# Kernel tuning notes

Measured on AMD Instinct MI355X. Metric: run time of the kernel, lower is better.

Reference implementation:

```python
import jax, jax.numpy as jnp
import numpy as np

B, S, D, H = 4, 1024, 1024, 16
DEPTH = D // H


def setup_inputs() -> dict:
    key = jax.random.key(0)
    ks = jax.random.split(key, 13)
    inp = {
        'query': jax.random.normal(ks[0], (B, S, D), dtype=jnp.float32),
        'key': jax.random.normal(ks[1], (B, S, D), dtype=jnp.float32),
        'value': jax.random.normal(ks[2], (B, S, D), dtype=jnp.float32),
        'mask': jax.random.bernoulli(ks[3], 0.1, (B, S, S)),
    }
    scale = 1.0 / np.sqrt(D)
    inp['wq_w'] = jax.random.uniform(ks[4], (D, D), jnp.float32, -scale, scale)
    inp['wq_b'] = jax.random.uniform(ks[5], (D,), jnp.float32, -scale, scale)
    inp['wk_w'] = jax.random.uniform(ks[6], (D, D), jnp.float32, -scale, scale)
    inp['wk_b'] = jax.random.uniform(ks[7], (D,), jnp.float32, -scale, scale)
    inp['wv_w'] = jax.random.uniform(ks[8], (D, D), jnp.float32, -scale, scale)
    inp['wv_b'] = jax.random.uniform(ks[9], (D,), jnp.float32, -scale, scale)
    inp['fc_w'] = jax.random.uniform(ks[10], (D, D), jnp.float32, -scale, scale)
    inp['fc_b'] = jax.random.uniform(ks[11], (D,), jnp.float32, -scale, scale)
    return inp


def _split_heads(x):
    # [B,S,D] -> [B,H,S,depth]
    b, s, _ = x.shape
    return x.reshape(b, s, H, DEPTH).transpose(0, 2, 1, 3)


def reference(query, key, value, mask, wq_w, wq_b, wk_w, wk_b, wv_w, wv_b, fc_w, fc_b):
    q = _split_heads(query @ wq_w.T + wq_b)
    k = _split_heads(key @ wk_w.T + wk_b)
    v = _split_heads(value @ wv_w.T + wv_b)
    scores = jnp.einsum('bhqd,bhkd->bhqk', q, k) / jnp.sqrt(jnp.float32(DEPTH))
    scores = jnp.where(mask[:, None, :, :], jnp.float32(-1e9), scores)
    attn = jax.nn.softmax(scores, axis=-1)
    out = jnp.einsum('bhqk,bhkd->bhqd', attn, v)  # [B,H,S,depth]
    out = out.transpose(0, 2, 1, 3).reshape(query.shape[0], -1, D)
    return out @ fc_w.T + fc_b
```

## Files before the change

kernel.cpp:

```cpp
#include <hip/hip_runtime.h>
#include <hip/hip_bf16.h>


typedef __bf16 bf16x8 __attribute__((ext_vector_type(8)));
typedef __bf16 bf16x4 __attribute__((ext_vector_type(4)));
typedef float  f32x4  __attribute__((ext_vector_type(4)));
typedef float  f32x16 __attribute__((ext_vector_type(16)));

typedef const __attribute__((address_space(1))) void* gptr_t;
typedef __attribute__((address_space(3))) void* lptr_t;

#define MFMA16(a, b, c) __builtin_amdgcn_mfma_f32_16x16x32_bf16((a), (b), (c), 0, 0, 0)
#define MFMA32(a, b, c) __builtin_amdgcn_mfma_f32_32x32x16_bf16((a), (b), (c), 0, 0, 0)

__device__ __forceinline__ void gload_lds16(const void* g, void* l) {
  __builtin_amdgcn_global_load_lds((gptr_t)g, (lptr_t)l, 16, 0, 0);
}

__device__ __forceinline__ unsigned pack2(float a, float b) {
  union { __bf16 h[2]; unsigned u; } x;
  x.h[0] = (__bf16)a; x.h[1] = (__bf16)b; return x.u;
}

__device__ __forceinline__ bf16x8 mkfrag(unsigned a, unsigned b, unsigned c, unsigned d) {
  union { unsigned w[4]; bf16x8 v; } x;
  x.w[0] = a; x.w[1] = b; x.w[2] = c; x.w[3] = d; return x.v;
}

__global__ void detect_mask(const unsigned char* m, int* flag) {
  __shared__ int s1[4], s23[4];
  int tid = threadIdx.x;
  uint4 v = ((const uint4*)m)[tid];
  unsigned x0 = v.x, x1 = v.y, x2 = v.z, x3 = v.w;
  unsigned c1  = (x0 & 0x0000ff00u) | (x1 & 0x0000ff00u) | (x2 & 0x0000ff00u) | (x3 & 0x0000ff00u);
  unsigned c23 = (x0 & 0xffff0000u) | (x1 & 0xffff0000u) | (x2 & 0xffff0000u) | (x3 & 0xffff0000u);
  unsigned long long b1 = __ballot(c1 != 0), b23 = __ballot(c23 != 0);
  if ((tid & 63) == 0) { s1[tid >> 6] = (b1 != 0); s23[tid >> 6] = (b23 != 0); }
  __syncthreads();
  if (tid == 0) {
    int a1 = s1[0] | s1[1] | s1[2] | s1[3];
    int a23 = s23[0] | s23[1] | s23[2] | s23[3];
    *flag = a1 ? 1 : (a23 ? 2 : 0);
  }
}

__global__ void pack_mask(const void* m, const int* flag, unsigned int* out) {
  size_t i = (size_t)blockIdx.x * 256 + threadIdx.x;
  int f = *flag;
  bool v;
  if (f == 1)      v = ((const unsigned char*)m)[i] != 0;
  else if (f == 2) v = ((const float*)m)[i] != 0.0f;
  else             v = ((const int*)m)[i] != 0;
  unsigned long long bal = __ballot(v);
  int lane = threadIdx.x & 63;
  if ((lane & 31) == 0) out[i >> 5] = (unsigned int)(bal >> (lane & 32));
}

__global__ void cvt_all(const float* q, const float* k, const float* v,
                        const float* w0, const float* w1, const float* w2, const float* w3,
                        __bf16* oq, __bf16* ok, __bf16* ov,
                        __bf16* o0, __bf16* o1, __bf16* o2, __bf16* o3) {
  int bid = blockIdx.x;
  const float* in; __bf16* out; int sub;
  if (bid < 12288) {
    int w = bid >> 12; sub = bid & 4095;
    in = w == 0 ? q : w == 1 ? k : v;
    out = w == 0 ? oq : w == 1 ? ok : ov;
  } else {
    int w = (bid - 12288) >> 10; sub = (bid - 12288) & 1023;
    in = w == 0 ? w0 : w == 1 ? w1 : w == 2 ? w2 : w3;
    out = w == 0 ? o0 : w == 1 ? o1 : w == 2 ? o2 : o3;
  }
  size_t i = (size_t)sub * 256 + threadIdx.x;
  float4 vv = ((const float4*)in)[i];
  bf16x4 o; o[0] = (__bf16)vv.x; o[1] = (__bf16)vv.y; o[2] = (__bf16)vv.z; o[3] = (__bf16)vv.w;
  ((bf16x4*)out)[i] = o;
}

__global__ __launch_bounds__(256, 2)
void gemm_qkv(const __bf16* __restrict__ qb, const __bf16* __restrict__ kb,
              const __bf16* __restrict__ vb,
              const __bf16* __restrict__ wq, const __bf16* __restrict__ wk,
              const __bf16* __restrict__ wv,
              const float* __restrict__ bq, const float* __restrict__ bk,
              const float* __restrict__ bv,
              __bf16* __restrict__ Qp, __bf16* __restrict__ Kp, __bf16* __restrict__ Vt) {
  __shared__ __bf16 As[2][128 * 64];
  __shared__ __bf16 Bs[2][128 * 64];
  const int bm = blockIdx.x;
  const int bnall = blockIdx.y;
  const int which = bnall >> 3;
  const int bn = bnall & 7;
  const __bf16* A = which == 0 ? qb : which == 1 ? kb : vb;
  const __bf16* W = which == 0 ? wq : which == 1 ? wk : wv;
  const float* bias = which == 0 ? bq : which == 1 ? bk : bv;

  const int tid = threadIdx.x, wave = tid >> 6, lane = tid & 63;
  const int wr = wave >> 1, wc = wave & 1;
  const int rl = lane >> 3, c8 = lane & 7;
  f32x4 acc[4][4] = {};

#define QKV_STAGE(bb, kt)                                                             \
  {                                                                                   \
    _Pragma("unroll")                                                                 \
    for (int i = 0; i < 4; ++i) {                                                     \
      int row = wave * 32 + i * 8 + rl;                                               \
      int sw = (c8 ^ (row & 7)) << 3;                                                 \
      gload_lds16(A + (size_t)(bm * 128 + row) * 1024 + (kt) * 64 + sw,               \
                  &As[bb][(wave * 32 + i * 8) * 64]);                                 \
      gload_lds16(W + (size_t)(bn * 128 + row) * 1024 + (kt) * 64 + sw,               \
                  &Bs[bb][(wave * 32 + i * 8) * 64]);                                 \
    }                                                                                 \
  }

  QKV_STAGE(0, 0);
  __syncthreads();
  int buf = 0;
  for (int kt = 0; kt < 16; ++kt) {
    if (kt < 15) QKV_STAGE(buf ^ 1, kt + 1);
#pragma unroll
    for (int k32 = 0; k32 < 2; ++k32) {
      bf16x8 af[4], bfr[4];
#pragma unroll
      for (int mi = 0; mi < 4; ++mi) {
        int row = wr * 64 + mi * 16 + (lane & 15);
        af[mi] = *(const bf16x8*)(&As[buf][row * 64 + (((k32 * 4 + (lane >> 4)) ^ (row & 7)) << 3)]);
      }
#pragma unroll
      for (int ni = 0; ni < 4; ++ni) {
        int row = wc * 64 + ni * 16 + (lane & 15);
        bfr[ni] = *(const bf16x8*)(&Bs[buf][row * 64 + (((k32 * 4 + (lane >> 4)) ^ (row & 7)) << 3)]);
      }
#pragma unroll
      for (int mi = 0; mi < 4; ++mi)
#pragma unroll
        for (int ni = 0; ni < 4; ++ni)
          acc[mi][ni] = MFMA16(af[mi], bfr[ni], acc[mi][ni]);
    }
    __syncthreads();
    buf ^= 1;
  }
  const int r0 = (lane >> 4) * 4, cl = lane & 15;
  const float osc = (which == 0) ? 0.18033688011112042f : 1.0f;
  __bf16* Onat = which == 0 ? Qp : Kp;
#pragma unroll
  for (int ni = 0; ni < 4; ++ni) {
    int col = bn * 128 + wc * 64 + ni * 16 + cl;
    float bvv = bias[col];
#pragma unroll
    for (int mi = 0; mi < 4; ++mi) {
      int rowb = bm * 128 + wr * 64 + mi * 16 + r0;
      if (which < 2) {
#pragma unroll
        for (int r = 0; r < 4; ++r)
          Onat[(size_t)(rowb + r) * 1024 + col] = (__bf16)((acc[mi][ni][r] + bvv) * osc);
      } else {
        int bb = rowb >> 10, s0 = rowb & 1023, hh = col >> 6, d = col & 63;
        bf16x4 ov;
#pragma unroll
        for (int r = 0; r < 4; ++r) ov[r] = (__bf16)(acc[mi][ni][r] + bvv);
        *(bf16x4*)(Vt + (((size_t)(bb * 16 + hh) * 64 + d) << 10) + s0) = ov;
      }
    }
  }
}

__global__ __launch_bounds__(256, 2)
void gemm_fc(const __bf16* __restrict__ A, const __bf16* __restrict__ W,
             const float* __restrict__ bias, float* __restrict__ C) {
  __shared__ __bf16 As[2][128 * 64];
  __shared__ __bf16 Bs[2][128 * 64];
  const int bm = blockIdx.x, bn = blockIdx.y;
  const int tid = threadIdx.x, wave = tid >> 6, lane = tid & 63;
  const int wr = wave >> 1, wc = wave & 1;
  const int rl = lane >> 3, c8 = lane & 7;
  f32x4 acc[4][4] = {};

#define FC_STAGE(bb, kt)                                                              \
  {                                                                                   \
    _Pragma("unroll")                                                                 \
    for (int i = 0; i < 4; ++i) {                                                     \
      int row = wave * 32 + i * 8 + rl;                                               \
      int sw = (c8 ^ (row & 7)) << 3;                                                 \
      gload_lds16(A + (size_t)(bm * 128 + row) * 1024 + (kt) * 64 + sw,               \
                  &As[bb][(wave * 32 + i * 8) * 64]);                                 \
      gload_lds16(W + (size_t)(bn * 128 + row) * 1024 + (kt) * 64 + sw,               \
                  &Bs[bb][(wave * 32 + i * 8) * 64]);                                 \
    }                                                                                 \
  }

  FC_STAGE(0, 0);
  __syncthreads();
  int buf = 0;
  for (int kt = 0; kt < 16; ++kt) {
    if (kt < 15) FC_STAGE(buf ^ 1, kt + 1);
#pragma unroll
    for (int k32 = 0; k32 < 2; ++k32) {
      bf16x8 af[4], bfr[4];
#pragma unroll
      for (int mi = 0; mi < 4; ++mi) {
        int row = wr * 64 + mi * 16 + (lane & 15);
        af[mi] = *(const bf16x8*)(&As[buf][row * 64 + (((k32 * 4 + (lane >> 4)) ^ (row & 7)) << 3)]);
      }
#pragma unroll
      for (int ni = 0; ni < 4; ++ni) {
        int row = wc * 64 + ni * 16 + (lane & 15);
        bfr[ni] = *(const bf16x8*)(&Bs[buf][row * 64 + (((k32 * 4 + (lane >> 4)) ^ (row & 7)) << 3)]);
      }
#pragma unroll
      for (int mi = 0; mi < 4; ++mi)
#pragma unroll
        for (int ni = 0; ni < 4; ++ni)
          acc[mi][ni] = MFMA16(af[mi], bfr[ni], acc[mi][ni]);
    }
    __syncthreads();
    buf ^= 1;
  }
  const int r0 = (lane >> 4) * 4, cl = lane & 15;
#pragma unroll
  for (int ni = 0; ni < 4; ++ni) {
    int col = bn * 128 + wc * 64 + ni * 16 + cl;
    float bvv = bias[col];
#pragma unroll
    for (int mi = 0; mi < 4; ++mi) {
      int rowb = bm * 128 + wr * 64 + mi * 16 + r0;
#pragma unroll
      for (int r = 0; r < 4; ++r)
        C[(size_t)(rowb + r) * 1024 + col] = acc[mi][ni][r] + bvv;
    }
  }
}

__global__ __launch_bounds__(256)
void attn32(const __bf16* __restrict__ Qp, const __bf16* __restrict__ Kp,
            const __bf16* __restrict__ Vt, const unsigned int* __restrict__ mp,
            __bf16* __restrict__ O) {
  __shared__ __bf16 Ks[2][64 * 64];
  __shared__ __bf16 Vs[2][64 * 64];
  const int tid = threadIdx.x, wave = tid >> 6, lane = tid & 63;
  const int lo5 = lane & 31, hi = lane >> 5;
  const int bx = blockIdx.x;
  const int qt = bx & 7, h = (bx >> 3) & 15, b = bx >> 7;
  const int qrow = qt * 128 + wave * 32 + lo5;

  const int srow = tid >> 3;
  const int sgx = ((tid & 7) ^ (srow & 7)) << 3;

#define ATTN_STAGE(bb, kt)                                                            \
  {                                                                                   \
    _Pragma("unroll")                                                                 \
    for (int i = 0; i < 2; ++i) {                                                     \
      gload_lds16(Kp + (size_t)(b * 1024 + (kt) * 64 + i * 32 + srow) * 1024          \
                     + h * 64 + sgx,                                                  \
                  &Ks[bb][i * 2048 + wave * 512]);                                    \
      gload_lds16(Vt + (size_t)((b * 16 + h) * 64 + i * 32 + srow) * 1024             \
                     + (kt) * 64 + sgx,                                               \
                  &Vs[bb][i * 2048 + wave * 512]);                                    \
    }                                                                                 \
  }

  bf16x8 qf[4];
  const __bf16* qb = Qp + ((size_t)(b * 1024 + qrow)) * 1024 + h * 64 + hi * 8;
#pragma unroll
  for (int m = 0; m < 4; ++m) qf[m] = *(const bf16x8*)(qb + m * 16);

  bf16x8 onesf;
#pragma unroll
  for (int i = 0; i < 8; ++i) onesf[i] = (__bf16)1.0f;

  f32x16 oacc0 = {}, oacc1 = {}, oaccD = {};
  const uint2* mrow = ((const uint2*)mp) + ((size_t)(b * 1024 + qrow)) * 16;
  const int x = lo5 & 7;

  ATTN_STAGE(0, 0);
  uint2 mwc = mrow[0];
  __syncthreads();
  int buf = 0;
  for (int kt = 0; kt < 16; ++kt) {
    if (kt < 15) ATTN_STAGE(buf ^ 1, kt + 1);
    uint2 mwn = mwc;
    if (kt < 15) mwn = mrow[kt + 1];
#pragma unroll
    for (int sub = 0; sub < 2; ++sub) {
      f32x16 s = {};
#pragma unroll
      for (int m = 0; m < 4; ++m) {
        bf16x8 kf = *(const bf16x8*)(&Ks[buf][(sub * 32 + lo5) * 64 + (((2 * m + hi) ^ x) << 3)]);
        s = MFMA32(kf, qf[m], s);
      }
      unsigned w32 = sub == 0 ? mwc.x : mwc.y;
      unsigned nw = ~(w32 >> (hi * 4));
      float p[16];
#pragma unroll
      for (int r = 0; r < 16; ++r) {
        float e = __builtin_amdgcn_exp2f(s[r]);
        unsigned keep = (unsigned)__builtin_amdgcn_sbfe((int)nw, (unsigned)((r & 3) + 8 * (r >> 2)), 1u);
        p[r] = __uint_as_float(__float_as_uint(e) & keep);
      }
      unsigned own[8];
#pragma unroll
      for (int u = 0; u < 4; ++u) {
        own[2 * u]     = pack2(p[4 * u],     p[4 * u + 1]);
        own[2 * u + 1] = pack2(p[4 * u + 2], p[4 * u + 3]);
      }
#pragma unroll
      for (int sf = 0; sf < 2; ++sf) {
        unsigned a0 = own[4 * sf + 0], b0 = own[4 * sf + 2];
        unsigned a1 = own[4 * sf + 1], b1 = own[4 * sf + 3];
        asm volatile("v_permlane32_swap_b32 %0, %1" : "+v"(a0), "+v"(b0));
        asm volatile("v_permlane32_swap_b32 %0, %1" : "+v"(a1), "+v"(b1));
        bf16x8 pa = mkfrag(a0, a1, b0, b1);
        int g = ((sub * 4 + sf * 2 + hi) ^ x) << 3;
        bf16x8 vf0 = *(const bf16x8*)(&Vs[buf][lo5 * 64 + g]);
        bf16x8 vf1 = *(const bf16x8*)(&Vs[buf][(lo5 + 32) * 64 + g]);
        oacc0 = MFMA32(pa, vf0, oacc0);
        oacc1 = MFMA32(pa, vf1, oacc1);
        oaccD = MFMA32(pa, onesf, oaccD);
      }
    }
    __syncthreads();
    buf ^= 1;
    mwc = mwn;
  }

  const size_t orow0 = (size_t)(b * 1024 + qt * 128 + wave * 32);
#pragma unroll
  for (int r = 0; r < 16; ++r) {
    int cr = (r & 3) + 8 * (r >> 2) + 4 * hi;
    float iv = __builtin_amdgcn_rcpf(oaccD[r]);
    __bf16* op = O + (orow0 + cr) * 1024 + h * 64 + lo5;
    op[0]  = (__bf16)(oacc0[r] * iv);
    op[32] = (__bf16)(oacc1[r] * iv);
  }
}

extern "C" void kernel_launch(void* const* d_in, const int* in_sizes, int n_in,
                              void* d_out, int out_size, void* d_ws, size_t ws_size,
                              hipStream_t stream) {
  const float* query = (const float*)d_in[0];
  const float* key   = (const float*)d_in[1];
  const float* value = (const float*)d_in[2];
  const void*  mask  = d_in[3];
  const float* wq_w  = (const float*)d_in[4];
  const float* wq_b  = (const float*)d_in[5];
  const float* wk_w  = (const float*)d_in[6];
  const float* wk_b  = (const float*)d_in[7];
  const float* wv_w  = (const float*)d_in[8];
  const float* wv_b  = (const float*)d_in[9];
  const float* fc_w  = (const float*)d_in[10];
  const float* fc_b  = (const float*)d_in[11];

  char* ws = (char*)d_ws;
  __bf16* qb  = (__bf16*)ws;
  __bf16* kb  = qb  + 4194304;
  __bf16* vb  = kb  + 4194304;
  __bf16* wqb = vb  + 4194304;
  __bf16* wkb = wqb + 1048576;
  __bf16* wvb = wkb + 1048576;
  __bf16* fcb = wvb + 1048576;
  __bf16* Qp  = fcb + 1048576;
  __bf16* Kp  = Qp  + 4194304;
  __bf16* Vt  = Kp  + 4194304;
  __bf16* Ob  = Vt  + 4194304;
  unsigned int* mpk = (unsigned int*)(Ob + 4194304);
  int* flag = (int*)(mpk + 131072);

  detect_mask<<<1, 256, 0, stream>>>((const unsigned char*)mask, flag);
  pack_mask<<<16384, 256, 0, stream>>>(mask, flag, mpk);
  cvt_all<<<16384, 256, 0, stream>>>(query, key, value, wq_w, wk_w, wv_w, fc_w,
                                     qb, kb, vb, wqb, wkb, wvb, fcb);
  dim3 g1(32, 24);
  gemm_qkv<<<g1, 256, 0, stream>>>(qb, kb, vb, wqb, wkb, wvb, wq_b, wk_b, wv_b, Qp, Kp, Vt);
  attn32<<<512, 256, 0, stream>>>(Qp, Kp, Vt, mpk, Ob);
  dim3 g2(32, 8);
  gemm_fc<<<g2, 256, 0, stream>>>(Ob, fcb, fc_b, (float*)d_out);
}
```

Measured before the change: 236.6 us.

## Rewrite QKV GEMM as 256x256 tile, 8-wave kernel with phased prefetch

Replaces the 128x128, 4-wave QKV projection GEMM with a 256x256 tile handled by 8 waves. The K loop is split into four compute phases, and each phase issues part of the next tile's global-to-LDS loads, with explicit barriers, sched_barrier and setprio around the MFMA bursts. The aim is more data reuse per block and better overlap of loads with MFMA work. The grid shrinks to 192 blocks, fewer than the CU count, so occupancy drops, and LDS use rises to 128KB per block.

```diff
diff --git a/kernel.cpp b/kernel.cpp
--- a/kernel.cpp
+++ b/kernel.cpp
@@ -77,79 +77,108 @@
   ((bf16x4*)out)[i] = o;
 }
 
-__global__ __launch_bounds__(256, 2)
-void gemm_qkv(const __bf16* __restrict__ qb, const __bf16* __restrict__ kb,
-              const __bf16* __restrict__ vb,
-              const __bf16* __restrict__ wq, const __bf16* __restrict__ wk,
-              const __bf16* __restrict__ wv,
-              const float* __restrict__ bq, const float* __restrict__ bk,
-              const float* __restrict__ bv,
-              __bf16* __restrict__ Qp, __bf16* __restrict__ Kp, __bf16* __restrict__ Vt) {
-  __shared__ __bf16 As[2][128 * 64];
-  __shared__ __bf16 Bs[2][128 * 64];
+__global__ __launch_bounds__(512, 2)
+void gemm_qkv8(const __bf16* __restrict__ qb, const __bf16* __restrict__ kb,
+               const __bf16* __restrict__ vb,
+               const __bf16* __restrict__ wq, const __bf16* __restrict__ wk,
+               const __bf16* __restrict__ wv,
+               const float* __restrict__ bq, const float* __restrict__ bk,
+               const float* __restrict__ bv,
+               __bf16* __restrict__ Qp, __bf16* __restrict__ Kp, __bf16* __restrict__ Vt) {
+  __shared__ __bf16 As[2][256 * 64];
+  __shared__ __bf16 Bs[2][256 * 64];
   const int bm = blockIdx.x;
   const int bnall = blockIdx.y;
-  const int which = bnall >> 3;
-  const int bn = bnall & 7;
+  const int which = bnall >> 2;
+  const int bnl = bnall & 3;
   const __bf16* A = which == 0 ? qb : which == 1 ? kb : vb;
   const __bf16* W = which == 0 ? wq : which == 1 ? wk : wv;
   const float* bias = which == 0 ? bq : which == 1 ? bk : bv;
 
   const int tid = threadIdx.x, wave = tid >> 6, lane = tid & 63;
-  const int wr = wave >> 1, wc = wave & 1;
-  const int rl = lane >> 3, c8 = lane & 7;
-  f32x4 acc[4][4] = {};
-
-#define QKV_STAGE(bb, kt)                                                             \
-  {                                                                                   \
-    _Pragma("unroll")                                                                 \
-    for (int i = 0; i < 4; ++i) {                                                     \
-      int row = wave * 32 + i * 8 + rl;                                               \
-      int sw = (c8 ^ (row & 7)) << 3;                                                 \
-      gload_lds16(A + (size_t)(bm * 128 + row) * 1024 + (kt) * 64 + sw,               \
-                  &As[bb][(wave * 32 + i * 8) * 64]);                                 \
-      gload_lds16(W + (size_t)(bn * 128 + row) * 1024 + (kt) * 64 + sw,               \
-                  &Bs[bb][(wave * 32 + i * 8) * 64]);                                 \
-    }                                                                                 \
-  }
-
-  QKV_STAGE(0, 0);
-  __syncthreads();
-  int buf = 0;
-  for (int kt = 0; kt < 16; ++kt) {
-    if (kt < 15) QKV_STAGE(buf ^ 1, kt + 1);
-#pragma unroll
-    for (int k32 = 0; k32 < 2; ++k32) {
-      bf16x8 af[4], bfr[4];
-#pragma unroll
-      for (int mi = 0; mi < 4; ++mi) {
-        int row = wr * 64 + mi * 16 + (lane & 15);
-        af[mi] = *(const bf16x8*)(&As[buf][row * 64 + (((k32 * 4 + (lane >> 4)) ^ (row & 7)) << 3)]);
-      }
-#pragma unroll
-      for (int ni = 0; ni < 4; ++ni) {
-        int row = wc * 64 + ni * 16 + (lane & 15);
-        bfr[ni] = *(const bf16x8*)(&Bs[buf][row * 64 + (((k32 * 4 + (lane >> 4)) ^ (row & 7)) << 3)]);
-      }
-#pragma unroll
-      for (int mi = 0; mi < 4; ++mi)
-#pragma unroll
-        for (int ni = 0; ni < 4; ++ni)
-          acc[mi][ni] = MFMA16(af[mi], bfr[ni], acc[mi][ni]);
-    }
-    __syncthreads();
-    buf ^= 1;
-  }
-  const int r0 = (lane >> 4) * 4, cl = lane & 15;
+  const int wr = wave >> 2, wc = wave & 3;
+  const int l15 = lane & 15, l4 = lane >> 4;
+  const int srow = tid >> 3;
+  const int sgw = ((tid & 7) ^ (srow & 7)) << 3;
+  f32x4 acc[8][4] = {};
+
+#define STAGE_HALF(bb, u, hp)                                                   \
+  {                                                                             \
+    _Pragma("unroll")                                                           \
+    for (int i_ = 0; i_ < 2; ++i_) {                                            \
+      int row_ = ((hp) & 1) * 128 + i_ * 64 + srow;                             \
+      if ((hp) < 2)                                                             \
+        gload_lds16(A + (size_t)(bm * 256 + row_) * 1024 + (u) * 64 + sgw,      \
+                    &As[bb][(((hp) & 1) * 128 + i_ * 64 + wave * 8) * 64]);     \
+      else                                                                      \
+        gload_lds16(W + (size_t)(bnl * 256 + row_) * 1024 + (u) * 64 + sgw,     \
+                    &Bs[bb][(((hp) & 1) * 128 + i_ * 64 + wave * 8) * 64]);     \
+    }                                                                           \
+  }
+
+#define PHASE(curb, mh, nh, DOSTAGE)                                            \
+  {                                                                             \
+    bf16x8 af_[4][2], bf_[2][2];                                                \
+    _Pragma("unroll")                                                           \
+    for (int j_ = 0; j_ < 4; ++j_) {                                            \
+      int row_ = wr * 128 + ((mh) * 4 + j_) * 16 + l15;                         \
+      _Pragma("unroll")                                                         \
+      for (int k_ = 0; k_ < 2; ++k_)                                            \
+        af_[j_][k_] = *(const bf16x8*)(&As[curb][row_ * 64 +                    \
+                          (((k_ * 4 + l4) ^ (row_ & 7)) << 3)]);                \
+    }                                                                           \
+    _Pragma("unroll")                                                           \
+    for (int n_ = 0; n_ < 2; ++n_) {                                            \
+      int row_ = wc * 64 + ((nh) * 2 + n_) * 16 + l15;                          \
+      _Pragma("unroll")                                                         \
+      for (int k_ = 0; k_ < 2; ++k_)                                            \
+        bf_[n_][k_] = *(const bf16x8*)(&Bs[curb][row_ * 64 +                    \
+                          (((k_ * 4 + l4) ^ (row_ & 7)) << 3)]);                \
+    }                                                                           \
+    DOSTAGE;                                                                    \
+    __builtin_amdgcn_s_barrier();                                               \
+    __builtin_amdgcn_sched_barrier(0);                                          \
+    __builtin_amdgcn_s_setprio(1);                                              \
+    _Pragma("unroll")                                                           \
+    for (int k_ = 0; k_ < 2; ++k_)                                              \
+      _Pragma("unroll")                                                         \
+      for (int j_ = 0; j_ < 4; ++j_)                                            \
+        _Pragma("unroll")                                                       \
+        for (int n_ = 0; n_ < 2; ++n_)                                          \
+          acc[(mh) * 4 + j_][(nh) * 2 + n_] =                                   \
+              MFMA16(af_[j_][k_], bf_[n_][k_], acc[(mh) * 4 + j_][(nh) * 2 + n_]); \
+    __builtin_amdgcn_s_setprio(0);                                              \
+    __builtin_amdgcn_s_barrier();                                               \
+    __builtin_amdgcn_sched_barrier(0);                                          \
+  }
+
+  STAGE_HALF(0, 0, 0); STAGE_HALF(0, 0, 1); STAGE_HALF(0, 0, 2); STAGE_HALF(0, 0, 3);
+  int cur = 0;
+#pragma unroll 1
+  for (int u = 0; u < 16; ++u) {
+    const int nu = u < 15 ? u + 1 : 15;
+    const int oth = cur ^ 1;
+    STAGE_HALF(oth, nu, 0);
+    asm volatile("s_waitcnt vmcnt(2)" ::: "memory");
+    __builtin_amdgcn_s_barrier();
+    __builtin_amdgcn_sched_barrier(0);
+    PHASE(cur, 0, 0, {});
+    PHASE(cur, 1, 0, STAGE_HALF(oth, nu, 1));
+    PHASE(cur, 0, 1, STAGE_HALF(oth, nu, 2));
+    PHASE(cur, 1, 1, STAGE_HALF(oth, nu, 3));
+    cur ^= 1;
+  }
+
+  const int r0 = l4 * 4, cl = l15;
   const float osc = (which == 0) ? 0.18033688011112042f : 1.0f;
   __bf16* Onat = which == 0 ? Qp : Kp;
 #pragma unroll
   for (int ni = 0; ni < 4; ++ni) {
-    int col = bn * 128 + wc * 64 + ni * 16 + cl;
+    int col = bnl * 256 + wc * 64 + ni * 16 + cl;
     float bvv = bias[col];
 #pragma unroll
-    for (int mi = 0; mi < 4; ++mi) {
-      int rowb = bm * 128 + wr * 64 + mi * 16 + r0;
+    for (int mi = 0; mi < 8; ++mi) {
+      int rowb = bm * 256 + wr * 128 + mi * 16 + r0;
       if (which < 2) {
 #pragma unroll
         for (int r = 0; r < 4; ++r)
@@ -163,6 +192,8 @@
       }
     }
   }
+#undef STAGE_HALF
+#undef PHASE
 }
 
 __global__ __launch_bounds__(256, 2)
@@ -369,8 +400,8 @@
   pack_mask<<<16384, 256, 0, stream>>>(mask, flag, mpk);
   cvt_all<<<16384, 256, 0, stream>>>(query, key, value, wq_w, wk_w, wv_w, fc_w,
                                      qb, kb, vb, wqb, wkb, wvb, fcb);
-  dim3 g1(32, 24);
-  gemm_qkv<<<g1, 256, 0, stream>>>(qb, kb, vb, wqb, wkb, wvb, wq_b, wk_b, wv_b, Qp, Kp, Vt);
+  dim3 g1(16, 12);
+  gemm_qkv8<<<g1, 512, 0, stream>>>(qb, kb, vb, wqb, wkb, wvb, wq_b, wk_b, wv_b, Qp, Kp, Vt);
   attn32<<<512, 256, 0, stream>>>(Qp, Kp, Vt, mpk, Ob);
   dim3 g2(32, 8);
   gemm_fc<<<g2, 256, 0, stream>>>(Ob, fcb, fc_b, (float*)d_out);
```

After: 240.7 us. About the same (+1.8%).

## Restructure GEMM main loops with two-stage-ahead prefetch and explicit waitcnt barriers

Applied to the files above, without the earlier changes.

Both projection GEMMs now issue loads two K-tiles ahead instead of one. They wait with explicit vmcnt counts rather than a full __syncthreads, so one tile's global-to-LDS loads stay in flight across the barrier. Each iteration reads all LDS fragments up front, barriers, refills the freed buffer, then runs the MFMAs at raised wave priority. The aim is to hide global memory latency behind compute. In exchange the schedule leans on hand-placed waitcnt values and sched_barriers, which are fragile if the load count per stage changes.

```diff
diff --git a/kernel.cpp b/kernel.cpp
--- a/kernel.cpp
+++ b/kernel.cpp
@@ -78,13 +78,13 @@
 }
 
 __global__ __launch_bounds__(256, 2)
-void gemm_qkv(const __bf16* __restrict__ qb, const __bf16* __restrict__ kb,
-              const __bf16* __restrict__ vb,
-              const __bf16* __restrict__ wq, const __bf16* __restrict__ wk,
-              const __bf16* __restrict__ wv,
-              const float* __restrict__ bq, const float* __restrict__ bk,
-              const float* __restrict__ bv,
-              __bf16* __restrict__ Qp, __bf16* __restrict__ Kp, __bf16* __restrict__ Vt) {
+void gemm_qkv2(const __bf16* __restrict__ qb, const __bf16* __restrict__ kb,
+               const __bf16* __restrict__ vb,
+               const __bf16* __restrict__ wq, const __bf16* __restrict__ wk,
+               const __bf16* __restrict__ wv,
+               const float* __restrict__ bq, const float* __restrict__ bk,
+               const float* __restrict__ bv,
+               __bf16* __restrict__ Qp, __bf16* __restrict__ Kp, __bf16* __restrict__ Vt) {
   __shared__ __bf16 As[2][128 * 64];
   __shared__ __bf16 Bs[2][128 * 64];
   const int bm = blockIdx.x;
@@ -97,50 +97,65 @@
 
   const int tid = threadIdx.x, wave = tid >> 6, lane = tid & 63;
   const int wr = wave >> 1, wc = wave & 1;
+  const int l15 = lane & 15, l4 = lane >> 4;
   const int rl = lane >> 3, c8 = lane & 7;
   f32x4 acc[4][4] = {};
 
 #define QKV_STAGE(bb, kt)                                                             \
   {                                                                                   \
     _Pragma("unroll")                                                                 \
-    for (int i = 0; i < 4; ++i) {                                                     \
-      int row = wave * 32 + i * 8 + rl;                                               \
-      int sw = (c8 ^ (row & 7)) << 3;                                                 \
-      gload_lds16(A + (size_t)(bm * 128 + row) * 1024 + (kt) * 64 + sw,               \
-                  &As[bb][(wave * 32 + i * 8) * 64]);                                 \
-      gload_lds16(W + (size_t)(bn * 128 + row) * 1024 + (kt) * 64 + sw,               \
-                  &Bs[bb][(wave * 32 + i * 8) * 64]);                                 \
+    for (int i_ = 0; i_ < 4; ++i_) {                                                  \
+      int row_ = wave * 32 + i_ * 8 + rl;                                             \
+      int sw_ = (c8 ^ (row_ & 7)) << 3;                                               \
+      gload_lds16(A + (size_t)(bm * 128 + row_) * 1024 + (kt) * 64 + sw_,             \
+                  &As[bb][(wave * 32 + i_ * 8) * 64]);                                \
+      gload_lds16(W + (size_t)(bn * 128 + row_) * 1024 + (kt) * 64 + sw_,             \
+                  &Bs[bb][(wave * 32 + i_ * 8) * 64]);                                \
     }                                                                                 \
   }
 
   QKV_STAGE(0, 0);
-  __syncthreads();
-  int buf = 0;
+  QKV_STAGE(1, 1);
+  int cur = 0;
+#pragma unroll 1
   for (int kt = 0; kt < 16; ++kt) {
-    if (kt < 15) QKV_STAGE(buf ^ 1, kt + 1);
-#pragma unroll
-    for (int k32 = 0; k32 < 2; ++k32) {
-      bf16x8 af[4], bfr[4];
-#pragma unroll
-      for (int mi = 0; mi < 4; ++mi) {
-        int row = wr * 64 + mi * 16 + (lane & 15);
-        af[mi] = *(const bf16x8*)(&As[buf][row * 64 + (((k32 * 4 + (lane >> 4)) ^ (row & 7)) << 3)]);
-      }
-#pragma unroll
-      for (int ni = 0; ni < 4; ++ni) {
-        int row = wc * 64 + ni * 16 + (lane & 15);
-        bfr[ni] = *(const bf16x8*)(&Bs[buf][row * 64 + (((k32 * 4 + (lane >> 4)) ^ (row & 7)) << 3)]);
-      }
+    if (kt < 15) asm volatile("s_waitcnt vmcnt(8)" ::: "memory");
+    else         asm volatile("s_waitcnt vmcnt(0)" ::: "memory");
+    __builtin_amdgcn_s_barrier();
+    __builtin_amdgcn_sched_barrier(0);
+    bf16x8 af[4][2], bfr[4][2];
+#pragma unroll
+    for (int mi = 0; mi < 4; ++mi) {
+      int row = wr * 64 + mi * 16 + l15;
+#pragma unroll
+      for (int k32 = 0; k32 < 2; ++k32)
+        af[mi][k32] = *(const bf16x8*)(&As[cur][row * 64 + (((k32 * 4 + l4) ^ (row & 7)) << 3)]);
+    }
+#pragma unroll
+    for (int ni = 0; ni < 4; ++ni) {
+      int row = wc * 64 + ni * 16 + l15;
+#pragma unroll
+      for (int k32 = 0; k32 < 2; ++k32)
+        bfr[ni][k32] = *(const bf16x8*)(&Bs[cur][row * 64 + (((k32 * 4 + l4) ^ (row & 7)) << 3)]);
+    }
+    asm volatile("s_waitcnt lgkmcnt(0)" ::: "memory");
+    __builtin_amdgcn_sched_barrier(0);
+    __builtin_amdgcn_s_barrier();
+    __builtin_amdgcn_sched_barrier(0);
+    if (kt < 14) QKV_STAGE(cur, kt + 2);
+    __builtin_amdgcn_s_setprio(1);
+#pragma unroll
+    for (int k32 = 0; k32 < 2; ++k32)
 #pragma unroll
       for (int mi = 0; mi < 4; ++mi)
 #pragma unroll
         for (int ni = 0; ni < 4; ++ni)
-          acc[mi][ni] = MFMA16(af[mi], bfr[ni], acc[mi][ni]);
-    }
-    __syncthreads();
-    buf ^= 1;
-  }
-  const int r0 = (lane >> 4) * 4, cl = lane & 15;
+          acc[mi][ni] = MFMA16(af[mi][k32], bfr[ni][k32], acc[mi][ni]);
+    __builtin_amdgcn_s_setprio(0);
+    cur ^= 1;
+  }
+
+  const int r0 = l4 * 4, cl = l15;
   const float osc = (which == 0) ? 0.18033688011112042f : 1.0f;
   __bf16* Onat = which == 0 ? Qp : Kp;
 #pragma unroll
@@ -163,6 +178,7 @@
       }
     }
   }
+#undef QKV_STAGE
 }
 
 __global__ __launch_bounds__(256, 2)
@@ -173,50 +189,64 @@
   const int bm = blockIdx.x, bn = blockIdx.y;
   const int tid = threadIdx.x, wave = tid >> 6, lane = tid & 63;
   const int wr = wave >> 1, wc = wave & 1;
+  const int l15 = lane & 15, l4 = lane >> 4;
   const int rl = lane >> 3, c8 = lane & 7;
   f32x4 acc[4][4] = {};
 
 #define FC_STAGE(bb, kt)                                                              \
   {                                                                                   \
     _Pragma("unroll")                                                                 \
-    for (int i = 0; i < 4; ++i) {                                                     \
-      int row = wave * 32 + i * 8 + rl;                                               \
-      int sw = (c8 ^ (row & 7)) << 3;                                                 \
-      gload_lds16(A + (size_t)(bm * 128 + row) * 1024 + (kt) * 64 + sw,               \
-                  &As[bb][(wave * 32 + i * 8) * 64]);                                 \
-      gload_lds16(W + (size_t)(bn * 128 + row) * 1024 + (kt) * 64 + sw,               \
-                  &Bs[bb][(wave * 32 + i * 8) * 64]);                                 \
+    for (int i_ = 0; i_ < 4; ++i_) {                                                  \
+      int row_ = wave * 32 + i_ * 8 + rl;                                             \
+      int sw_ = (c8 ^ (row_ & 7)) << 3;                                               \
+      gload_lds16(A + (size_t)(bm * 128 + row_) * 1024 + (kt) * 64 + sw_,             \
+                  &As[bb][(wave * 32 + i_ * 8) * 64]);                                \
+      gload_lds16(W + (size_t)(bn * 128 + row_) * 1024 + (kt) * 64 + sw_,             \
+                  &Bs[bb][(wave * 32 + i_ * 8) * 64]);                                \
     }                                                                                 \
   }
 
   FC_STAGE(0, 0);
-  __syncthreads();
-  int buf = 0;
+  FC_STAGE(1, 1);
+  int cur = 0;
+#pragma unroll 1
   for (int kt = 0; kt < 16; ++kt) {
-    if (kt < 15) FC_STAGE(buf ^ 1, kt + 1);
-#pragma unroll
-    for (int k32 = 0; k32 < 2; ++k32) {
-      bf16x8 af[4], bfr[4];
-#pragma unroll
-      for (int mi = 0; mi < 4; ++mi) {
-        int row = wr * 64 + mi * 16 + (lane & 15);
-        af[mi] = *(const bf16x8*)(&As[buf][row * 64 + (((k32 * 4 + (lane >> 4)) ^ (row & 7)) << 3)]);
-      }
-#pragma unroll
-      for (int ni = 0; ni < 4; ++ni) {
-        int row = wc * 64 + ni * 16 + (lane & 15);
-        bfr[ni] = *(const bf16x8*)(&Bs[buf][row * 64 + (((k32 * 4 + (lane >> 4)) ^ (row & 7)) << 3)]);
-      }
+    if (kt < 15) asm volatile("s_waitcnt vmcnt(8)" ::: "memory");
+    else         asm volatile("s_waitcnt vmcnt(0)" ::: "memory");
+    __builtin_amdgcn_s_barrier();
+    __builtin_amdgcn_sched_barrier(0);
+    bf16x8 af[4][2], bfr[4][2];
+#pragma unroll
+    for (int mi = 0; mi < 4; ++mi) {
+      int row = wr * 64 + mi * 16 + l15;
+#pragma unroll
+      for (int k32 = 0; k32 < 2; ++k32)
+        af[mi][k32] = *(const bf16x8*)(&As[cur][row * 64 + (((k32 * 4 + l4) ^ (row & 7)) << 3)]);
+    }
+#pragma unroll
+    for (int ni = 0; ni < 4; ++ni) {
+      int row = wc * 64 + ni * 16 + l15;
+#pragma unroll
+      for (int k32 = 0; k32 < 2; ++k32)
+        bfr[ni][k32] = *(const bf16x8*)(&Bs[cur][row * 64 + (((k32 * 4 + l4) ^ (row & 7)) << 3)]);
+    }
+    asm volatile("s_waitcnt lgkmcnt(0)" ::: "memory");
+    __builtin_amdgcn_sched_barrier(0);
+    __builtin_amdgcn_s_barrier();
+    __builtin_amdgcn_sched_barrier(0);
+    if (kt < 14) FC_STAGE(cur, kt + 2);
+    __builtin_amdgcn_s_setprio(1);
+#pragma unroll
+    for (int k32 = 0; k32 < 2; ++k32)
 #pragma unroll
       for (int mi = 0; mi < 4; ++mi)
 #pragma unroll
         for (int ni = 0; ni < 4; ++ni)
-          acc[mi][ni] = MFMA16(af[mi], bfr[ni], acc[mi][ni]);
-    }
-    __syncthreads();
-    buf ^= 1;
-  }
-  const int r0 = (lane >> 4) * 4, cl = lane & 15;
+          acc[mi][ni] = MFMA16(af[mi][k32], bfr[ni][k32], acc[mi][ni]);
+    __builtin_amdgcn_s_setprio(0);
+    cur ^= 1;
+  }
+  const int r0 = l4 * 4, cl = l15;
 #pragma unroll
   for (int ni = 0; ni < 4; ++ni) {
     int col = bn * 128 + wc * 64 + ni * 16 + cl;
@@ -229,6 +259,7 @@
         C[(size_t)(rowb + r) * 1024 + col] = acc[mi][ni][r] + bvv;
     }
   }
+#undef FC_STAGE
 }
 
 __global__ __launch_bounds__(256)
@@ -332,6 +363,7 @@
     op[0]  = (__bf16)(oacc0[r] * iv);
     op[32] = (__bf16)(oacc1[r] * iv);
   }
+#undef ATTN_STAGE
 }
 
 extern "C" void kernel_launch(void* const* d_in, const int* in_sizes, int n_in,
@@ -370,7 +402,7 @@
   cvt_all<<<16384, 256, 0, stream>>>(query, key, value, wq_w, wk_w, wv_w, fc_w,
                                      qb, kb, vb, wqb, wkb, wvb, fcb);
   dim3 g1(32, 24);
-  gemm_qkv<<<g1, 256, 0, stream>>>(qb, kb, vb, wqb, wkb, wvb, wq_b, wk_b, wv_b, Qp, Kp, Vt);
+  gemm_qkv2<<<g1, 256, 0, stream>>>(qb, kb, vb, wqb, wkb, wvb, wq_b, wk_b, wv_b, Qp, Kp, Vt);
   attn32<<<512, 256, 0, stream>>>(Qp, Kp, Vt, mpk, Ob);
   dim3 g2(32, 8);
   gemm_fc<<<g2, 256, 0, stream>>>(Ob, fcb, fc_b, (float*)d_out);
```

After: 226.2 us. 4.4% less time.
